# Optimization experiments

Measured on AMD Instinct MI355X. Metric: run time of the kernel, lower is better.

## Reference

```python
import jax, jax.numpy as jnp
import numpy as np

B, NPG, H, D = 8, 6250, 4, 128   # graphs, nodes/graph, heads, hidden
N = B * NPG                       # 50000 nodes total
E = 400000                        # edges
VOCAB = 10000


def setup_inputs() -> dict:
    key = jax.random.key(0)
    ks = jax.random.split(key, 12)
    p = lambda k, shape: jax.random.normal(k, shape, dtype=jnp.float32) * 0.05
    return {
        "node_ids": jax.random.randint(ks[0], (N,), 0, VOCAB),
        "src": jax.random.randint(ks[1], (E,), 0, N),
        "dst": jax.random.randint(ks[2], (E,), 0, N),
        "emb": p(ks[3], (VOCAB, D)),
        "W_src": p(ks[4], (D, H * D)), "b_src": jnp.zeros((H * D,), jnp.float32),
        "W_dst": p(ks[5], (D, H * D)), "b_dst": jnp.zeros((H * D,), jnp.float32),
        "attn": p(ks[6], (H, D)),
        "W_res": p(ks[7], (D, H * D)), "b_res": jnp.zeros((H * D,), jnp.float32),
        "W_gc": p(ks[8], (D, D)), "b_gc": jnp.zeros((D,), jnp.float32),
        "W_mlp": p(ks[9], (3 * D, 1)), "b_mlp": jnp.zeros((1,), jnp.float32),
    }


def _leaky(x, s):
    return jnp.where(x >= 0, x, s * x)


def _maxpool(feat):
    # dgl.max_nodes: per-graph max over nodes -> [B, feat_dim]
    return jnp.max(feat.reshape(B, NPG, -1), axis=1)


def _gatv2(x, src, dst, W_src, b_src, W_dst, b_dst, attn, W_res, b_res):
    # DGL GATv2Conv (share_weights=False, residual=True, eval mode -> no dropout)
    hs = (x @ W_src + b_src).reshape(N, H, D)
    hd = (x @ W_dst + b_dst).reshape(N, H, D)
    e = _leaky(hs[src] + hd[dst], 0.2)              # [E,H,D]
    logits = jnp.einsum('ehd,hd->eh', e, attn)      # [E,H]
    m = jax.ops.segment_max(logits, dst, num_segments=N)
    ex = jnp.exp(logits - m[dst])
    denom = jax.ops.segment_sum(ex, dst, num_segments=N)
    alpha = ex / denom[dst]                          # edge softmax per dst/head
    rst = jax.ops.segment_sum(hs[src] * alpha[..., None], dst, num_segments=N)
    rst = rst + (x @ W_res + b_res).reshape(N, H, D)
    return _leaky(rst, 0.01)                         # nn.LeakyReLU() activation


def _graphconv(x, src, dst, W, b):
    # DGL GraphConv norm='both', allow_zero_in_degree=True, LeakyReLU activation
    ones = jnp.ones((E,), x.dtype)
    dout = jnp.clip(jax.ops.segment_sum(ones, src, num_segments=N), 1.0, None)
    din = jnp.clip(jax.ops.segment_sum(ones, dst, num_segments=N), 1.0, None)
    h = x * jax.lax.rsqrt(dout)[:, None]
    agg = jax.ops.segment_sum(h[src], dst, num_segments=N)
    h = agg * jax.lax.rsqrt(din)[:, None]
    return _leaky(h @ W + b, 0.01)


def reference(node_ids, src, dst, emb, W_src, b_src, W_dst, b_dst, attn,
              W_res, b_res, W_gc, b_gc, W_mlp, b_mlp):
    feat = emb[node_ids]                             # featurize_nodes
    pools = [_maxpool(feat)]
    res = _gatv2(feat, src, dst, W_src, b_src, W_dst, b_dst, attn,
                 W_res, b_res).mean(axis=1)          # mean over heads -> [N,D]
    pools.append(_maxpool(res))
    res = _graphconv(res, src, dst, W_gc, b_gc)
    pools.append(_maxpool(res))
    agg = jnp.concatenate(pools, axis=1)             # [B, 3D]
    # reward_predictor_block_two: ReLU -> (Dropout eval) -> Linear(3D, 1)
    return jax.nn.relu(agg) @ W_mlp + b_mlp          # BCE logits [B,1]
```

## Files before the change

kernel.cpp:

```cpp
#include <hip/hip_runtime.h>
#include <float.h>
#include <math.h>

#define Bg   8
#define NPGc 6250
#define Hh   4
#define Dd   128
#define Nn   50000
#define Ee   400000
#define HDd  512
#define WNf  1536
#define NCHUNK 49

typedef unsigned short ushort_t;
typedef __attribute__((ext_vector_type(8))) short bf16x8;
typedef __attribute__((ext_vector_type(4))) float f32x4;
typedef __attribute__((ext_vector_type(2))) float f32x2;

__device__ __forceinline__ void atomicMaxF(float* addr, float val) {
    if (val >= 0.0f) atomicMax((int*)addr, __float_as_int(val));
    else             atomicMin((unsigned int*)addr, __float_as_uint(val));
}

__device__ __forceinline__ ushort_t f2bf(float x) {
    unsigned u = __float_as_uint(x);
    unsigned r = (u + 0x7FFFu + ((u >> 16) & 1u)) >> 16;
    return (ushort_t)r;
}

__device__ __forceinline__ f32x2 bfpair(unsigned u) {
    f32x2 r;
    r.x = __uint_as_float(u << 16);
    r.y = __uint_as_float(u & 0xFFFF0000u);
    return r;
}

__global__ void setup_kernel(const int* __restrict__ ids, const float* __restrict__ emb,
                             float* __restrict__ feat, ushort_t* __restrict__ feat_bf,
                             const float* __restrict__ W_src, const float* __restrict__ W_dst,
                             const float* __restrict__ W_res, const float* __restrict__ W_gc,
                             const float* __restrict__ b_src, const float* __restrict__ b_dst,
                             const float* __restrict__ b_res,
                             ushort_t* __restrict__ Wt, ushort_t* __restrict__ Wt_gc,
                             float* __restrict__ bias_f,
                             int* __restrict__ din_i, float* __restrict__ dout,
                             int* __restrict__ cursor, float* __restrict__ pools) {
    int i = blockIdx.x * blockDim.x + threadIdx.x;
    {
        int n = i >> 5, c = i & 31;
        int id = ids[n];
        float4 v = ((const float4*)emb)[(size_t)id * 32 + c];
        ((float4*)feat)[(size_t)n * 32 + c] = v;
        ushort4 b;
        b.x = f2bf(v.x); b.y = f2bf(v.y); b.z = f2bf(v.z); b.w = f2bf(v.w);
        ((ushort4*)feat_bf)[(size_t)n * 32 + c] = b;
    }
    if (i < Nn) { din_i[i] = 0; dout[i] = 0.0f; cursor[i] = 0; }
    if (i < Bg * 3 * Dd) pools[i] = -FLT_MAX;
    if (i < WNf * 128) {
        int c = i >> 7, k = i & 127;
        float v = (c < 512) ? W_src[k * 512 + c]
                : (c < 1024) ? W_dst[k * 512 + (c - 512)]
                             : W_res[k * 512 + (c - 1024)];
        Wt[i] = f2bf(v);
    } else if (i < WNf * 128 + 128 * 128) {
        int j = i - WNf * 128;
        int c = j >> 7, k = j & 127;
        Wt_gc[j] = f2bf(W_gc[k * 128 + c]);
    }
    if (i < WNf)
        bias_f[i] = (i < 512) ? b_src[i] : (i < 1024) ? b_dst[i - 512] : b_res[i - 1024];
}

__global__ void maxpool_kernel(const float* __restrict__ x, float* __restrict__ pools, int col_off) {
    int b = blockIdx.x, chunk = blockIdx.y, d = threadIdx.x;
    int i0 = chunk * 125, i1 = i0 + 125;
    float mx = -FLT_MAX;
    for (int i = i0; i < i1; ++i)
        mx = fmaxf(mx, x[((size_t)(b * NPGc + i)) * Dd + d]);
    atomicMaxF(&pools[b * (3 * Dd) + col_off + d], mx);
}

#define GNT 3
__global__ __launch_bounds__(256) void mfma_gemm_kernel(
    const ushort_t* __restrict__ A, const ushort_t* __restrict__ Wt,
    const float* __restrict__ bias, ushort_t* __restrict__ Ob,
    int n_rows, int WN)
{
    __shared__ ushort_t Cs[2][64 * 64];
    int ct0   = blockIdx.y * GNT;
    int row0  = blockIdx.x * 64;
    int w = threadIdx.x >> 6, lane = threadIdx.x & 63;
    int lrow = lane & 15, kg = lane >> 4;

    bf16x8 av[4][4];
    {
        const ushort_t* ap = A + (size_t)(row0 + lrow) * 128 + kg * 8;
        #pragma unroll
        for (int fi = 0; fi < 4; ++fi)
            #pragma unroll
            for (int ks = 0; ks < 4; ++ks)
                av[fi][ks] = *(const bf16x8*)(ap + fi * 16 * 128 + ks * 32);
    }
    bf16x8 wv[GNT][4];
    float4 bv[GNT];
    {
        const ushort_t* wp = Wt + (size_t)(ct0 * 64 + w * 16 + lrow) * 128 + kg * 8;
        #pragma unroll
        for (int ct = 0; ct < GNT; ++ct) {
            #pragma unroll
            for (int ks = 0; ks < 4; ++ks)
                wv[ct][ks] = *(const bf16x8*)(wp + (size_t)ct * 8192 + ks * 32);
            bv[ct] = *(const float4*)(bias + (ct0 + ct) * 64 + w * 16 + kg * 4);
        }
    }

    #pragma unroll
    for (int ct = 0; ct < GNT; ++ct) {
        f32x4 acc[4] = {};
        #pragma unroll
        for (int ks = 0; ks < 4; ++ks)
            #pragma unroll
            for (int fi = 0; fi < 4; ++fi)
                acc[fi] = __builtin_amdgcn_mfma_f32_16x16x32_bf16(wv[ct][ks], av[fi][ks], acc[fi], 0, 0, 0);

        ushort_t* cb = Cs[ct & 1];
        int cbase = w * 32 + kg * 8;
        #pragma unroll
        for (int fi = 0; fi < 4; ++fi) {
            float o0 = acc[fi][0] + bv[ct].x;
            float o1 = acc[fi][1] + bv[ct].y;
            float o2 = acc[fi][2] + bv[ct].z;
            float o3 = acc[fi][3] + bv[ct].w;
            unsigned q0, q1;
            asm("v_cvt_pk_bf16_f32 %0, %1, %2" : "=v"(q0) : "v"(o0), "v"(o1));
            asm("v_cvt_pk_bf16_f32 %0, %1, %2" : "=v"(q1) : "v"(o2), "v"(o3));
            int r = fi * 16 + lrow;
            int cbyte = cbase ^ ((r & 7) << 4);
            uint2 q; q.x = q0; q.y = q1;
            *(uint2*)((char*)cb + r * 128 + cbyte) = q;
        }
        __syncthreads();
        {
            int t = threadIdx.x;
            const char* cbr = (const char*)cb;
            #pragma unroll
            for (int h = 0; h < 2; ++h) {
                int r  = (h * 256 + t) >> 3;
                int ch = t & 7;
                int cbyte = (ch * 16) ^ ((r & 7) << 4);
                uint4 v = *(const uint4*)(cbr + r * 128 + cbyte);
                int grow = row0 + r;
                if (grow < n_rows)
                    *(uint4*)((char*)Ob + ((size_t)grow * WN + (ct0 + ct) * 64) * 2 + ch * 16) = v;
            }
        }
    }
}

__global__ __launch_bounds__(256) void mfma_gc_pool_kernel(
    const ushort_t* __restrict__ A, const ushort_t* __restrict__ Wt,
    const float* __restrict__ bias, float* __restrict__ pools)
{
    int g = blockIdx.x / 98, lb = blockIdx.x % 98;
    int row0 = g * NPGc + lb * 64;
    int w = threadIdx.x >> 6, lane = threadIdx.x & 63;
    int lrow = lane & 15, kg = lane >> 4;

    bf16x8 av[4][4];
    {
        const ushort_t* ap = A + (size_t)(row0 + lrow) * 128 + kg * 8;
        #pragma unroll
        for (int fi = 0; fi < 4; ++fi)
            #pragma unroll
            for (int ks = 0; ks < 4; ++ks)
                av[fi][ks] = *(const bf16x8*)(ap + fi * 16 * 128 + ks * 32);
    }

    #pragma unroll
    for (int ct = 0; ct < 2; ++ct) {
        bf16x8 wv[4];
        const ushort_t* wp = Wt + (size_t)(ct * 64 + w * 16 + lrow) * 128 + kg * 8;
        #pragma unroll
        for (int ks = 0; ks < 4; ++ks) wv[ks] = *(const bf16x8*)(wp + ks * 32);

        f32x4 acc[4] = {};
        #pragma unroll
        for (int ks = 0; ks < 4; ++ks)
            #pragma unroll
            for (int fi = 0; fi < 4; ++fi)
                acc[fi] = __builtin_amdgcn_mfma_f32_16x16x32_bf16(wv[ks], av[fi][ks], acc[fi], 0, 0, 0);

        int colb = ct * 64 + w * 16 + kg * 4;
        float4 bv4 = *(const float4*)(bias + colb);
        float mcol[4] = {-FLT_MAX, -FLT_MAX, -FLT_MAX, -FLT_MAX};
        #pragma unroll
        for (int fi = 0; fi < 4; ++fi) {
            int lr = lb * 64 + fi * 16 + lrow;
            bool valid = lr < NPGc;
            #pragma unroll
            for (int j = 0; j < 4; ++j) {
                float v = acc[fi][j] + ((const float*)&bv4)[j];
                v = v >= 0.0f ? v : 0.01f * v;
                if (valid) mcol[j] = fmaxf(mcol[j], v);
            }
        }
        #pragma unroll
        for (int j = 0; j < 4; ++j) {
            mcol[j] = fmaxf(mcol[j], __shfl_xor(mcol[j], 1));
            mcol[j] = fmaxf(mcol[j], __shfl_xor(mcol[j], 2));
            mcol[j] = fmaxf(mcol[j], __shfl_xor(mcol[j], 4));
            mcol[j] = fmaxf(mcol[j], __shfl_xor(mcol[j], 8));
        }
        if (lrow == 0) {
            #pragma unroll
            for (int j = 0; j < 4; ++j)
                atomicMaxF(&pools[g * (3 * Dd) + 2 * Dd + colb + j], mcol[j]);
        }
    }
}

__global__ void degree2_kernel(const int* __restrict__ src, const int* __restrict__ dst,
                               int* __restrict__ din_i, float* __restrict__ dout) {
    int e = blockIdx.x * blockDim.x + threadIdx.x;
    if (e >= Ee) return;
    atomicAdd(&din_i[dst[e]], 1);
    atomicAdd(&dout[src[e]], 1.0f);
}

__global__ __launch_bounds__(256) void scan_reduce_kernel(const int* __restrict__ din_i,
                                                          int* __restrict__ partials) {
    int b = blockIdx.x, t = threadIdx.x;
    int base = b * 1024 + t * 4;
    int s = 0;
    #pragma unroll
    for (int j = 0; j < 4; ++j) { int i = base + j; if (i < Nn) s += din_i[i]; }
    #pragma unroll
    for (int off = 32; off > 0; off >>= 1) s += __shfl_xor(s, off);
    __shared__ int wsum[4];
    if ((t & 63) == 0) wsum[t >> 6] = s;
    __syncthreads();
    if (t == 0) partials[b] = wsum[0] + wsum[1] + wsum[2] + wsum[3];
}

__global__ void scan_mid_kernel(int* __restrict__ partials, int* __restrict__ row_start) {
    if (threadIdx.x == 0) {
        int acc = 0;
        for (int i = 0; i < NCHUNK; ++i) { int v = partials[i]; partials[i] = acc; acc += v; }
        row_start[Nn] = acc;
    }
}

__global__ __launch_bounds__(256) void scan_final_kernel(const int* __restrict__ din_i,
                                                         const int* __restrict__ partials,
                                                         int* __restrict__ row_start,
                                                         float* __restrict__ din_f) {
    int b = blockIdx.x, t = threadIdx.x;
    int base = b * 1024 + t * 4;
    int v[4]; int s = 0;
    #pragma unroll
    for (int j = 0; j < 4; ++j) {
        v[j] = (base + j < Nn) ? din_i[base + j] : 0;
        s += v[j];
    }
    __shared__ int buf[256];
    buf[t] = s;
    __syncthreads();
    #pragma unroll
    for (int off = 1; off < 256; off <<= 1) {
        int x = (t >= off) ? buf[t - off] : 0;
        __syncthreads();
        buf[t] += x;
        __syncthreads();
    }
    int excl = buf[t] - s + partials[b];
    #pragma unroll
    for (int j = 0; j < 4; ++j) {
        if (base + j < Nn) {
            row_start[base + j] = excl;
            din_f[base + j] = (float)v[j];
            excl += v[j];
        }
    }
}

__global__ void scatter_kernel(const int* __restrict__ src, const int* __restrict__ dst,
                               const int* __restrict__ row_start, int* __restrict__ cursor,
                               int* __restrict__ csr_src) {
    int e = blockIdx.x * blockDim.x + threadIdx.x;
    if (e >= Ee) return;
    int d = dst[e];
    int slot = row_start[d] + atomicAdd(&cursor[d], 1);
    csr_src[slot] = src[e];
}

__global__ __launch_bounds__(256) void gat_fused_kernel(
    const ushort_t* __restrict__ h_all, const float* __restrict__ attn,
    const int* __restrict__ row_start, const int* __restrict__ csr_src,
    float* __restrict__ res, ushort_t* __restrict__ res_bf)
{
    int d = (blockIdx.x * 256 + threadIdx.x) >> 6;
    int lane = threadIdx.x & 63;
    if (d >= Nn) return;
    int e0 = row_start[d], e1 = row_start[d + 1];

    const f32x2 z2 = {0.0f, 0.0f};
    f32x2 hd0, hd1, hd2, hd3, at0, at1, at2, at3;
    {
        uint4 hr = *(const uint4*)(h_all + (size_t)d * WNf + 512 + lane * 8);
        hd0 = bfpair(hr.x); hd1 = bfpair(hr.y); hd2 = bfpair(hr.z); hd3 = bfpair(hr.w);
        float4 a0 = *(const float4*)(attn + lane * 8);
        float4 a1 = *(const float4*)(attn + lane * 8 + 4);
        at0.x = a0.x; at0.y = a0.y; at1.x = a0.z; at1.y = a0.w;
        at2.x = a1.x; at2.y = a1.y; at3.x = a1.z; at3.y = a1.w;
    }

    float denom = 0.0f;
    f32x2 ac0 = z2, ac1 = z2, ac2 = z2, ac3 = z2;

    int s0 = (e0 < e1) ? csr_src[e0] : 0;
    int s1 = (e0 + 1 < e1) ? csr_src[e0 + 1] : s0;
    uint4 r0 = *(const uint4*)(h_all + (size_t)s0 * WNf + lane * 8);
    uint4 r1 = *(const uint4*)(h_all + (size_t)s1 * WNf + lane * 8);
    for (int e = e0; e < e1; ++e) {
        int s2 = (e + 2 < e1) ? csr_src[e + 2] : s0;
        uint4 r2 = *(const uint4*)(h_all + (size_t)s2 * WNf + lane * 8);
        f32x2 h0 = bfpair(r0.x), h1 = bfpair(r0.y), h2 = bfpair(r0.z), h3 = bfpair(r0.w);
        f32x2 p2 = z2;
        {
            f32x2 x = h0 + hd0;
            f32x2 lk = __builtin_elementwise_max(x, z2) + 0.2f * __builtin_elementwise_min(x, z2);
            p2 += lk * at0;
        }
        {
            f32x2 x = h1 + hd1;
            f32x2 lk = __builtin_elementwise_max(x, z2) + 0.2f * __builtin_elementwise_min(x, z2);
            p2 += lk * at1;
        }
        {
            f32x2 x = h2 + hd2;
            f32x2 lk = __builtin_elementwise_max(x, z2) + 0.2f * __builtin_elementwise_min(x, z2);
            p2 += lk * at2;
        }
        {
            f32x2 x = h3 + hd3;
            f32x2 lk = __builtin_elementwise_max(x, z2) + 0.2f * __builtin_elementwise_min(x, z2);
            p2 += lk * at3;
        }
        float p = p2.x + p2.y;
        p += __shfl_xor(p, 1); p += __shfl_xor(p, 2);
        p += __shfl_xor(p, 4); p += __shfl_xor(p, 8);
        p = fminf(fmaxf(p, -40.0f), 40.0f);
        float ex = __expf(p);
        denom += ex;
        ac0 += h0 * ex; ac1 += h1 * ex; ac2 += h2 * ex; ac3 += h3 * ex;
        r0 = r1; r1 = r2;
    }

    float inv = (e1 > e0) ? 1.0f / denom : 0.0f;
    f32x2 rv0, rv1, rv2, rv3;
    {
        uint4 rr = *(const uint4*)(h_all + (size_t)d * WNf + 1024 + lane * 8);
        rv0 = bfpair(rr.x); rv1 = bfpair(rr.y); rv2 = bfpair(rr.z); rv3 = bfpair(rr.w);
    }
    float t[8];
    {
        f32x2 v0 = ac0 * inv + rv0, v1 = ac1 * inv + rv1;
        f32x2 v2 = ac2 * inv + rv2, v3 = ac3 * inv + rv3;
        f32x2 l0 = __builtin_elementwise_max(v0, z2) + 0.01f * __builtin_elementwise_min(v0, z2);
        f32x2 l1 = __builtin_elementwise_max(v1, z2) + 0.01f * __builtin_elementwise_min(v1, z2);
        f32x2 l2 = __builtin_elementwise_max(v2, z2) + 0.01f * __builtin_elementwise_min(v2, z2);
        f32x2 l3 = __builtin_elementwise_max(v3, z2) + 0.01f * __builtin_elementwise_min(v3, z2);
        t[0] = l0.x; t[1] = l0.y; t[2] = l1.x; t[3] = l1.y;
        t[4] = l2.x; t[5] = l2.y; t[6] = l3.x; t[7] = l3.y;
    }
    #pragma unroll
    for (int j = 0; j < 8; ++j) {
        t[j] += __shfl_xor(t[j], 16);
        t[j] += __shfl_xor(t[j], 32);
    }
    if (lane < 16) {
        float o0[4] = {0.25f * t[0], 0.25f * t[1], 0.25f * t[2], 0.25f * t[3]};
        float o1[4] = {0.25f * t[4], 0.25f * t[5], 0.25f * t[6], 0.25f * t[7]};
        *(float4*)(res + (size_t)d * Dd + lane * 8)     = *(float4*)o0;
        *(float4*)(res + (size_t)d * Dd + lane * 8 + 4) = *(float4*)o1;
        unsigned q0, q1, q2, q3;
        asm("v_cvt_pk_bf16_f32 %0, %1, %2" : "=v"(q0) : "v"(o0[0]), "v"(o0[1]));
        asm("v_cvt_pk_bf16_f32 %0, %1, %2" : "=v"(q1) : "v"(o0[2]), "v"(o0[3]));
        asm("v_cvt_pk_bf16_f32 %0, %1, %2" : "=v"(q2) : "v"(o1[0]), "v"(o1[1]));
        asm("v_cvt_pk_bf16_f32 %0, %1, %2" : "=v"(q3) : "v"(o1[2]), "v"(o1[3]));
        uint4 qb; qb.x = q0; qb.y = q1; qb.z = q2; qb.w = q3;
        *(uint4*)(res_bf + (size_t)d * Dd + lane * 8) = qb;
    }
}

__global__ __launch_bounds__(256) void gc_gather_kernel(
    const ushort_t* __restrict__ res_bf, const int* __restrict__ row_start,
    const int* __restrict__ csr_src, const float* __restrict__ dout,
    const float* __restrict__ din, ushort_t* __restrict__ agg_bf)
{
    int d = (blockIdx.x * 256 + threadIdx.x) >> 6;
    int lane = threadIdx.x & 63;
    if (d >= Nn) return;
    int e0 = row_start[d], e1 = row_start[d + 1];
    const f32x2 z2 = {0.0f, 0.0f};
    f32x2 a2 = z2;
    int s0 = (e0 < e1) ? csr_src[e0] : 0;
    int s1 = (e0 + 1 < e1) ? csr_src[e0 + 1] : s0;
    float sc0 = 1.0f / sqrtf(fmaxf((e0 < e1) ? dout[s0] : 1.0f, 1.0f));
    float sc1 = 1.0f / sqrtf(fmaxf((e0 + 1 < e1) ? dout[s1] : 1.0f, 1.0f));
    unsigned u0 = *(const unsigned*)(res_bf + (size_t)s0 * Dd + lane * 2);
    unsigned u1 = *(const unsigned*)(res_bf + (size_t)s1 * Dd + lane * 2);
    for (int e = e0; e < e1; ++e) {
        int s2 = (e + 2 < e1) ? csr_src[e + 2] : s0;
        float sc2 = 1.0f / sqrtf(fmaxf(dout[s2], 1.0f));
        unsigned u2 = *(const unsigned*)(res_bf + (size_t)s2 * Dd + lane * 2);
        a2 += bfpair(u0) * sc0;
        u0 = u1; u1 = u2; sc0 = sc1; sc1 = sc2;
    }
    float scd = 1.0f / sqrtf(fmaxf(din[d], 1.0f));
    float ax = a2.x * scd, ay = a2.y * scd;
    unsigned q;
    asm("v_cvt_pk_bf16_f32 %0, %1, %2" : "=v"(q) : "v"(ax), "v"(ay));
    *(unsigned*)(agg_bf + (size_t)d * Dd + lane * 2) = q;
}

__global__ void final_kernel(const float* __restrict__ pools, const float* __restrict__ W_mlp,
                             const float* __restrict__ b_mlp, float* __restrict__ out) {
    int b = blockIdx.x, lane = threadIdx.x;
    float s = 0.0f;
    for (int j = lane; j < 3 * Dd; j += 64)
        s += fmaxf(pools[b * (3 * Dd) + j], 0.0f) * W_mlp[j];
    #pragma unroll
    for (int off = 32; off > 0; off >>= 1) s += __shfl_xor(s, off);
    if (lane == 0) out[b] = s + b_mlp[0];
}

extern "C" void kernel_launch(void* const* d_in, const int* in_sizes, int n_in,
                              void* d_out, int out_size, void* d_ws, size_t ws_size,
                              hipStream_t stream) {
    const int*   node_ids = (const int*)d_in[0];
    const int*   src      = (const int*)d_in[1];
    const int*   dst      = (const int*)d_in[2];
    const float* emb      = (const float*)d_in[3];
    const float* W_src    = (const float*)d_in[4];
    const float* b_src    = (const float*)d_in[5];
    const float* W_dst    = (const float*)d_in[6];
    const float* b_dst    = (const float*)d_in[7];
    const float* attn     = (const float*)d_in[8];
    const float* W_res    = (const float*)d_in[9];
    const float* b_res    = (const float*)d_in[10];
    const float* W_gc     = (const float*)d_in[11];
    const float* b_gc     = (const float*)d_in[12];
    const float* W_mlp    = (const float*)d_in[13];
    const float* b_mlp    = (const float*)d_in[14];
    float* out = (float*)d_out;

    char* w = (char*)d_ws;
    size_t off = 0;
    float*    feat    = (float*)(w + off);    off += (size_t)Nn * Dd * 4;
    ushort_t* feat_bf = (ushort_t*)(w + off); off += (size_t)(Nn + 64) * Dd * 2;
    ushort_t* h_all   = (ushort_t*)(w + off); off += (size_t)Nn * WNf * 2;
    ushort_t* Wt      = (ushort_t*)(w + off); off += (size_t)WNf * 128 * 2;
    ushort_t* Wt_gc   = (ushort_t*)(w + off); off += (size_t)128 * 128 * 2;
    float*    bias_f  = (float*)(w + off);    off += (size_t)WNf * 4;
    int*      csr_src = (int*)(w + off);      off += (size_t)Ee * 4;
    int*      row_st  = (int*)(w + off);      off += ((size_t)Nn + 4) * 4;
    int*      cursor  = (int*)(w + off);      off += (size_t)Nn * 4;
    int*      din_i   = (int*)(w + off);      off += (size_t)Nn * 4;
    float*    din_f   = (float*)(w + off);    off += (size_t)Nn * 4;
    float*    dout_f  = (float*)(w + off);    off += (size_t)Nn * 4;
    int*      partials= (int*)(w + off);      off += 64 * 4;
    float*    pools   = (float*)(w + off);    off += (size_t)Bg * 3 * Dd * 4;
    ushort_t* res_bf  = (ushort_t*)(w + off); off += (size_t)Nn * Dd * 2;

    float*    res    = feat;
    ushort_t* agg_bf = h_all;

    setup_kernel<<<(Nn * 32) / 256, 256, 0, stream>>>(
        node_ids, emb, feat, feat_bf, W_src, W_dst, W_res, W_gc,
        b_src, b_dst, b_res, Wt, Wt_gc, bias_f, din_i, dout_f, cursor, pools);
    maxpool_kernel<<<dim3(Bg, 50), Dd, 0, stream>>>(feat, pools, 0);

    degree2_kernel<<<(Ee + 255) / 256, 256, 0, stream>>>(src, dst, din_i, dout_f);
    scan_reduce_kernel<<<NCHUNK, 256, 0, stream>>>(din_i, partials);
    scan_mid_kernel<<<1, 64, 0, stream>>>(partials, row_st);
    scan_final_kernel<<<NCHUNK, 256, 0, stream>>>(din_i, partials, row_st, din_f);
    scatter_kernel<<<(Ee + 255) / 256, 256, 0, stream>>>(src, dst, row_st, cursor, csr_src);

    mfma_gemm_kernel<<<dim3((Nn + 63) / 64, 8), 256, 0, stream>>>(
        feat_bf, Wt, bias_f, h_all, Nn, WNf);

    gat_fused_kernel<<<(Nn * 64) / 256, 256, 0, stream>>>(h_all, attn, row_st, csr_src, res, res_bf);
    maxpool_kernel<<<dim3(Bg, 50), Dd, 0, stream>>>(res, pools, Dd);

    gc_gather_kernel<<<(Nn * 64) / 256, 256, 0, stream>>>(res_bf, row_st, csr_src, dout_f, din_f, agg_bf);
    mfma_gc_pool_kernel<<<Bg * 98, 256, 0, stream>>>(agg_bf, Wt_gc, b_gc, pools);

    final_kernel<<<Bg, 64, 0, stream>>>(pools, W_mlp, b_mlp, out);
}
```

Before: 393.4 us.

## Unroll GAT edge loop by four, drop fp32 res write, swizzle GEMM blocks

```diff
diff --git a/kernel.cpp b/kernel.cpp
--- a/kernel.cpp
+++ b/kernel.cpp
@@ -81,6 +81,18 @@
     atomicMaxF(&pools[b * (3 * Dd) + col_off + d], mx);
 }
 
+__global__ void maxpool_bf_kernel(const ushort_t* __restrict__ x, float* __restrict__ pools, int col_off) {
+    int b = blockIdx.x, chunk = blockIdx.y, lane = threadIdx.x;
+    int i0 = chunk * 125;
+    f32x2 mx = {-FLT_MAX, -FLT_MAX};
+    for (int i = 0; i < 125; ++i) {
+        unsigned u = *(const unsigned*)(x + ((size_t)(b * NPGc + i0 + i)) * Dd + lane * 2);
+        mx = __builtin_elementwise_max(mx, bfpair(u));
+    }
+    atomicMaxF(&pools[b * (3 * Dd) + col_off + lane * 2],     mx.x);
+    atomicMaxF(&pools[b * (3 * Dd) + col_off + lane * 2 + 1], mx.y);
+}
+
 #define GNT 3
 __global__ __launch_bounds__(256) void mfma_gemm_kernel(
     const ushort_t* __restrict__ A, const ushort_t* __restrict__ Wt,
@@ -88,8 +100,10 @@
     int n_rows, int WN)
 {
     __shared__ ushort_t Cs[2][64 * 64];
-    int ct0   = blockIdx.y * GNT;
-    int row0  = blockIdx.x * 64;
+    int bid = blockIdx.x;
+    int lin = (bid & 7) * (gridDim.x >> 3) + (bid >> 3);
+    int row0 = (lin >> 3) * 64;
+    int ct0  = (lin & 7) * GNT;
     int w = threadIdx.x >> 6, lane = threadIdx.x & 63;
     int lrow = lane & 15, kg = lane >> 4;
 
@@ -297,7 +311,7 @@
 __global__ __launch_bounds__(256) void gat_fused_kernel(
     const ushort_t* __restrict__ h_all, const float* __restrict__ attn,
     const int* __restrict__ row_start, const int* __restrict__ csr_src,
-    float* __restrict__ res, ushort_t* __restrict__ res_bf)
+    ushort_t* __restrict__ res_bf)
 {
     int d = (blockIdx.x * 256 + threadIdx.x) >> 6;
     int lane = threadIdx.x & 63;
@@ -318,44 +332,62 @@
     float denom = 0.0f;
     f32x2 ac0 = z2, ac1 = z2, ac2 = z2, ac3 = z2;
 
-    int s0 = (e0 < e1) ? csr_src[e0] : 0;
-    int s1 = (e0 + 1 < e1) ? csr_src[e0 + 1] : s0;
-    uint4 r0 = *(const uint4*)(h_all + (size_t)s0 * WNf + lane * 8);
-    uint4 r1 = *(const uint4*)(h_all + (size_t)s1 * WNf + lane * 8);
-    for (int e = e0; e < e1; ++e) {
-        int s2 = (e + 2 < e1) ? csr_src[e + 2] : s0;
-        uint4 r2 = *(const uint4*)(h_all + (size_t)s2 * WNf + lane * 8);
-        f32x2 h0 = bfpair(r0.x), h1 = bfpair(r0.y), h2 = bfpair(r0.z), h3 = bfpair(r0.w);
-        f32x2 p2 = z2;
-        {
-            f32x2 x = h0 + hd0;
-            f32x2 lk = __builtin_elementwise_max(x, z2) + 0.2f * __builtin_elementwise_min(x, z2);
-            p2 += lk * at0;
-        }
-        {
-            f32x2 x = h1 + hd1;
-            f32x2 lk = __builtin_elementwise_max(x, z2) + 0.2f * __builtin_elementwise_min(x, z2);
-            p2 += lk * at1;
-        }
-        {
-            f32x2 x = h2 + hd2;
-            f32x2 lk = __builtin_elementwise_max(x, z2) + 0.2f * __builtin_elementwise_min(x, z2);
-            p2 += lk * at2;
-        }
-        {
-            f32x2 x = h3 + hd3;
-            f32x2 lk = __builtin_elementwise_max(x, z2) + 0.2f * __builtin_elementwise_min(x, z2);
-            p2 += lk * at3;
-        }
-        float p = p2.x + p2.y;
+#define LOGIT_PRE(r, h0, h1, h2, h3, pout)                                            \
+    {                                                                                 \
+        h0 = bfpair(r.x); h1 = bfpair(r.y); h2 = bfpair(r.z); h3 = bfpair(r.w);       \
+        f32x2 p2 = z2;                                                                \
+        { f32x2 x = h0 + hd0;                                                         \
+          p2 += (__builtin_elementwise_max(x, z2) + 0.2f * __builtin_elementwise_min(x, z2)) * at0; } \
+        { f32x2 x = h1 + hd1;                                                         \
+          p2 += (__builtin_elementwise_max(x, z2) + 0.2f * __builtin_elementwise_min(x, z2)) * at1; } \
+        { f32x2 x = h2 + hd2;                                                         \
+          p2 += (__builtin_elementwise_max(x, z2) + 0.2f * __builtin_elementwise_min(x, z2)) * at2; } \
+        { f32x2 x = h3 + hd3;                                                         \
+          p2 += (__builtin_elementwise_max(x, z2) + 0.2f * __builtin_elementwise_min(x, z2)) * at3; } \
+        pout = p2.x + p2.y;                                                           \
+    }
+
+    int e = e0;
+    for (; e + 4 <= e1; e += 4) {
+        int sA = csr_src[e], sB = csr_src[e + 1], sC = csr_src[e + 2], sD = csr_src[e + 3];
+        uint4 rA = *(const uint4*)(h_all + (size_t)sA * WNf + lane * 8);
+        uint4 rB = *(const uint4*)(h_all + (size_t)sB * WNf + lane * 8);
+        uint4 rC = *(const uint4*)(h_all + (size_t)sC * WNf + lane * 8);
+        uint4 rD = *(const uint4*)(h_all + (size_t)sD * WNf + lane * 8);
+        f32x2 hA0, hA1, hA2, hA3, hB0, hB1, hB2, hB3;
+        f32x2 hC0, hC1, hC2, hC3, hD0, hD1, hD2, hD3;
+        float pA, pB, pC, pD;
+        LOGIT_PRE(rA, hA0, hA1, hA2, hA3, pA);
+        LOGIT_PRE(rB, hB0, hB1, hB2, hB3, pB);
+        LOGIT_PRE(rC, hC0, hC1, hC2, hC3, pC);
+        LOGIT_PRE(rD, hD0, hD1, hD2, hD3, pD);
+        pA += __shfl_xor(pA, 1); pB += __shfl_xor(pB, 1); pC += __shfl_xor(pC, 1); pD += __shfl_xor(pD, 1);
+        pA += __shfl_xor(pA, 2); pB += __shfl_xor(pB, 2); pC += __shfl_xor(pC, 2); pD += __shfl_xor(pD, 2);
+        pA += __shfl_xor(pA, 4); pB += __shfl_xor(pB, 4); pC += __shfl_xor(pC, 4); pD += __shfl_xor(pD, 4);
+        pA += __shfl_xor(pA, 8); pB += __shfl_xor(pB, 8); pC += __shfl_xor(pC, 8); pD += __shfl_xor(pD, 8);
+        float exA = __expf(fminf(fmaxf(pA, -40.0f), 40.0f));
+        float exB = __expf(fminf(fmaxf(pB, -40.0f), 40.0f));
+        float exC = __expf(fminf(fmaxf(pC, -40.0f), 40.0f));
+        float exD = __expf(fminf(fmaxf(pD, -40.0f), 40.0f));
+        denom += (exA + exB) + (exC + exD);
+        ac0 += hA0 * exA + hB0 * exB + hC0 * exC + hD0 * exD;
+        ac1 += hA1 * exA + hB1 * exB + hC1 * exC + hD1 * exD;
+        ac2 += hA2 * exA + hB2 * exB + hC2 * exC + hD2 * exD;
+        ac3 += hA3 * exA + hB3 * exB + hC3 * exC + hD3 * exD;
+    }
+    for (; e < e1; ++e) {
+        int s = csr_src[e];
+        uint4 r = *(const uint4*)(h_all + (size_t)s * WNf + lane * 8);
+        f32x2 h0, h1, h2, h3;
+        float p;
+        LOGIT_PRE(r, h0, h1, h2, h3, p);
         p += __shfl_xor(p, 1); p += __shfl_xor(p, 2);
         p += __shfl_xor(p, 4); p += __shfl_xor(p, 8);
-        p = fminf(fmaxf(p, -40.0f), 40.0f);
-        float ex = __expf(p);
+        float ex = __expf(fminf(fmaxf(p, -40.0f), 40.0f));
         denom += ex;
         ac0 += h0 * ex; ac1 += h1 * ex; ac2 += h2 * ex; ac3 += h3 * ex;
-        r0 = r1; r1 = r2;
-    }
+    }
+#undef LOGIT_PRE
 
     float inv = (e1 > e0) ? 1.0f / denom : 0.0f;
     f32x2 rv0, rv1, rv2, rv3;
@@ -380,15 +412,13 @@
         t[j] += __shfl_xor(t[j], 32);
     }
     if (lane < 16) {
-        float o0[4] = {0.25f * t[0], 0.25f * t[1], 0.25f * t[2], 0.25f * t[3]};
-        float o1[4] = {0.25f * t[4], 0.25f * t[5], 0.25f * t[6], 0.25f * t[7]};
-        *(float4*)(res + (size_t)d * Dd + lane * 8)     = *(float4*)o0;
-        *(float4*)(res + (size_t)d * Dd + lane * 8 + 4) = *(float4*)o1;
+        float o0 = 0.25f * t[0], o1 = 0.25f * t[1], o2 = 0.25f * t[2], o3 = 0.25f * t[3];
+        float o4 = 0.25f * t[4], o5 = 0.25f * t[5], o6 = 0.25f * t[6], o7 = 0.25f * t[7];
         unsigned q0, q1, q2, q3;
-        asm("v_cvt_pk_bf16_f32 %0, %1, %2" : "=v"(q0) : "v"(o0[0]), "v"(o0[1]));
-        asm("v_cvt_pk_bf16_f32 %0, %1, %2" : "=v"(q1) : "v"(o0[2]), "v"(o0[3]));
-        asm("v_cvt_pk_bf16_f32 %0, %1, %2" : "=v"(q2) : "v"(o1[0]), "v"(o1[1]));
-        asm("v_cvt_pk_bf16_f32 %0, %1, %2" : "=v"(q3) : "v"(o1[2]), "v"(o1[3]));
+        asm("v_cvt_pk_bf16_f32 %0, %1, %2" : "=v"(q0) : "v"(o0), "v"(o1));
+        asm("v_cvt_pk_bf16_f32 %0, %1, %2" : "=v"(q1) : "v"(o2), "v"(o3));
+        asm("v_cvt_pk_bf16_f32 %0, %1, %2" : "=v"(q2) : "v"(o4), "v"(o5));
+        asm("v_cvt_pk_bf16_f32 %0, %1, %2" : "=v"(q3) : "v"(o6), "v"(o7));
         uint4 qb; qb.x = q0; qb.y = q1; qb.z = q2; qb.w = q3;
         *(uint4*)(res_bf + (size_t)d * Dd + lane * 8) = qb;
     }
@@ -474,7 +504,6 @@
     float*    pools   = (float*)(w + off);    off += (size_t)Bg * 3 * Dd * 4;
     ushort_t* res_bf  = (ushort_t*)(w + off); off += (size_t)Nn * Dd * 2;
 
-    float*    res    = feat;
     ushort_t* agg_bf = h_all;
 
     setup_kernel<<<(Nn * 32) / 256, 256, 0, stream>>>(
@@ -488,11 +517,11 @@
     scan_final_kernel<<<NCHUNK, 256, 0, stream>>>(din_i, partials, row_st, din_f);
     scatter_kernel<<<(Ee + 255) / 256, 256, 0, stream>>>(src, dst, row_st, cursor, csr_src);
 
-    mfma_gemm_kernel<<<dim3((Nn + 63) / 64, 8), 256, 0, stream>>>(
+    mfma_gemm_kernel<<<((Nn + 63) / 64) * 8, 256, 0, stream>>>(
         feat_bf, Wt, bias_f, h_all, Nn, WNf);
 
-    gat_fused_kernel<<<(Nn * 64) / 256, 256, 0, stream>>>(h_all, attn, row_st, csr_src, res, res_bf);
-    maxpool_kernel<<<dim3(Bg, 50), Dd, 0, stream>>>(res, pools, Dd);
+    gat_fused_kernel<<<(Nn * 64) / 256, 256, 0, stream>>>(h_all, attn, row_st, csr_src, res_bf);
+    maxpool_bf_kernel<<<dim3(Bg, 50), 64, 0, stream>>>(res_bf, pools, Dd);
 
     gc_gather_kernel<<<(Nn * 64) / 256, 256, 0, stream>>>(res_bf, row_st, csr_src, dout_f, din_f, agg_bf);
     mfma_gc_pool_kernel<<<Bg * 98, 256, 0, stream>>>(agg_bf, Wt_gc, b_gc, pools);
```

After: 374.1 us. 4.9% less time.
